# Kernel optimization log

Hardware: AMD Instinct MI355X
Metric: run time of the kernel (lower is better)

## Reference

```python
import jax, jax.numpy as jnp
import numpy as np

DIM = 2048
N_HEADS = 16
Q_LORA = 1536
KV_LORA = 512
NOPE = 128
ROPE = 64
V_DIM = 128
QK_HEAD = NOPE + ROPE
SEQ = 4096
THETA = 10000.0
EPS = 1e-6
SCALE = QK_HEAD ** -0.5  # max_seq_len==4096 not >4096, so no mscale adjustment


def rms_norm(x, w):
    return x * jax.lax.rsqrt(jnp.mean(x * x, axis=-1, keepdims=True) + EPS) * w


def rope_cos_sin(seqlen):
    inv_freq = 1.0 / THETA ** (jnp.arange(0, ROPE, 2, dtype=jnp.float32) / ROPE)  # [ROPE/2]
    t = jnp.arange(seqlen, dtype=jnp.float32)
    freqs = jnp.outer(t, inv_freq)  # [S, ROPE/2]
    return jnp.cos(freqs), jnp.sin(freqs)


def apply_rope(x, cos, sin):
    # x: (b, s, h, ROPE); pairs (x0, x1) rotated as complex mult, interleaved layout
    b, s, h, d = x.shape
    xr = x.reshape(b, s, h, d // 2, 2)
    x0, x1 = xr[..., 0], xr[..., 1]
    c = cos[None, :, None, :]
    sn = sin[None, :, None, :]
    out = jnp.stack([x0 * c - x1 * sn, x0 * sn + x1 * c], axis=-1)
    return out.reshape(b, s, h, d)


def setup_inputs() -> dict:
    key = jax.random.key(0)
    ks = jax.random.split(key, 8)
    s = lambda fan_in: 1.0 / np.sqrt(fan_in)
    return {
        "x": jax.random.normal(ks[0], (1, SEQ, DIM), jnp.float32),
        "wq_a_w": jax.random.normal(ks[1], (Q_LORA, DIM), jnp.float32) * s(DIM),
        "q_norm_w": 1.0 + 0.02 * jax.random.normal(ks[2], (Q_LORA,), jnp.float32),
        "wq_b_w": jax.random.normal(ks[3], (N_HEADS * QK_HEAD, Q_LORA), jnp.float32) * s(Q_LORA),
        "wkv_a_w": jax.random.normal(ks[4], (KV_LORA + ROPE, DIM), jnp.float32) * s(DIM),
        "kv_norm_w": 1.0 + 0.02 * jax.random.normal(ks[5], (KV_LORA,), jnp.float32),
        "wkv_b_w": jax.random.normal(ks[6], (N_HEADS * (NOPE + V_DIM), KV_LORA), jnp.float32) * s(KV_LORA),
        "wo_w": jax.random.normal(ks[7], (DIM, DIM), jnp.float32) * s(DIM),
    }


def reference(x, wq_a_w, q_norm_w, wq_b_w, wkv_a_w, kv_norm_w, wkv_b_w, wo_w):
    b, seqlen, _ = x.shape
    cos, sin = rope_cos_sin(seqlen)

    # Q path: low-rank down-proj -> RMSNorm -> up-proj
    q = rms_norm(x @ wq_a_w.T, q_norm_w) @ wq_b_w.T
    q = q.reshape(b, seqlen, N_HEADS, QK_HEAD)
    q_nope, q_pe = q[..., :NOPE], q[..., NOPE:]
    q_pe = apply_rope(q_pe, cos, sin)

    # KV path: compressed latent + decoupled rope key
    kv_a = x @ wkv_a_w.T  # (b, s, KV_LORA + ROPE)
    kv_latent, k_pe_raw = kv_a[..., :KV_LORA], kv_a[..., KV_LORA:]
    kv = rms_norm(kv_latent, kv_norm_w)               # (b, t, c)
    k_pe = apply_rope(k_pe_raw[:, :, None, :], cos, sin)[:, :, 0, :]  # (b, t, r)

    # Absorption trick: fold wkv_b's K-part into q_nope, attend against latents
    wkv_b = wkv_b_w.reshape(N_HEADS, NOPE + V_DIM, KV_LORA)
    q_abs = jnp.einsum("bshd,hdc->bshc", q_nope, wkv_b[:, :NOPE])

    scores = (jnp.einsum("bshc,btc->bsht", q_abs, kv)
              + jnp.einsum("bshr,btr->bsht", q_pe, k_pe)) * SCALE

    # causal additive mask over (s_query, t_key)
    causal = jnp.tril(jnp.ones((seqlen, seqlen), dtype=bool))
    scores = jnp.where(causal[None, :, None, :], scores, jnp.float32(-1e30))
    attn = jax.nn.softmax(scores, axis=-1)

    # post-softmax: aggregate latents, then recover V via wkv_b's V-part
    ctx = jnp.einsum("bsht,btc->bshc", attn, kv)
    v = jnp.einsum("bshc,hdc->bshd", ctx, wkv_b[:, NOPE:])  # (b, s, h, V_DIM)
    out = v.reshape(b, seqlen, N_HEADS * V_DIM) @ wo_w.T
    return out
```

## Files before the change

### kernel.cpp

```cpp
#include <hip/hip_runtime.h>

typedef unsigned short u16;
typedef __attribute__((ext_vector_type(8))) short bf16x8;
typedef __attribute__((ext_vector_type(4))) float f32x4;
typedef __attribute__((ext_vector_type(4))) unsigned short u16x4;

#define MFMA16(a, b, c) __builtin_amdgcn_mfma_f32_16x16x32_bf16((a), (b), (c), 0, 0, 0)

#define SEQ 4096
#define SCALE 0.07216878364870323f
#define LOGTHETA 9.210340371976184f

__device__ __forceinline__ u16 f2bf(float f) {
  union { float f; unsigned u; } c; c.f = f;
  unsigned u = c.u;
  unsigned r = (u + 0x7fffu + ((u >> 16) & 1u)) >> 16;
  return (u16)r;
}
__device__ __forceinline__ float bf2f(u16 b) {
  union { unsigned u; float f; } c; c.u = ((unsigned)b) << 16;
  return c.f;
}

__global__ void cvt_all(const float* __restrict__ x, const float* __restrict__ wqa,
                        const float* __restrict__ wqb, const float* __restrict__ wkva,
                        const float* __restrict__ wkvb, const float* __restrict__ wo,
                        u16* __restrict__ xb, u16* __restrict__ wqab,
                        u16* __restrict__ wqbb, u16* __restrict__ wkvab,
                        u16* __restrict__ wkvbb, u16* __restrict__ wob) {
  const int e0 = 2097152;
  const int e1 = e0 + 786432;
  const int e2 = e1 + 1179648;
  const int e3 = e2 + 294912;
  const int e4 = e3 + 524288;
  const int e5 = e4 + 1048576;
  int stride = gridDim.x * blockDim.x;
  for (int i = blockIdx.x * blockDim.x + threadIdx.x; i < e5; i += stride) {
    const float* src; u16* dst; int j;
    if (i < e0)      { src = x;    dst = xb;    j = i; }
    else if (i < e1) { src = wqa;  dst = wqab;  j = i - e0; }
    else if (i < e2) { src = wqb;  dst = wqbb;  j = i - e1; }
    else if (i < e3) { src = wkva; dst = wkvab; j = i - e2; }
    else if (i < e4) { src = wkvb; dst = wkvbb; j = i - e3; }
    else             { src = wo;   dst = wob;   j = i - e4; }
    f32x4 v = ((const f32x4*)src)[j];
    u16x4 o;
    o[0] = f2bf(v[0]); o[1] = f2bf(v[1]); o[2] = f2bf(v[2]); o[3] = f2bf(v[3]);
    ((u16x4*)dst)[j] = o;
  }
}

__global__ void trans_wkvb(const float* __restrict__ w, u16* __restrict__ wt) {
  __shared__ float tile[64][65];
  int c0 = blockIdx.x * 64;
  int d0 = blockIdx.y * 64;
  int h = blockIdx.z;
  for (int k = 0; k < 16; k++) {
    int el = threadIdx.x + k * 256;
    int r = el >> 6, c = el & 63;
    tile[r][c] = w[(h * 256 + d0 + r) * 512 + c0 + c];
  }
  __syncthreads();
  for (int k = 0; k < 16; k++) {
    int el = threadIdx.x + k * 256;
    int r = el >> 6, c = el & 63;
    wt[h * 65536 + (c0 + r) * 128 + d0 + c] = f2bf(tile[c][r]);
  }
}

__global__ void trans_vt(const u16* __restrict__ cc, u16* __restrict__ vt2) {
  __shared__ u16 tile[64][65];
  int c0 = blockIdx.x * 64;
  int t0 = blockIdx.y * 64;
  for (int k = 0; k < 16; k++) {
    int el = threadIdx.x + k * 256;
    int r = el >> 6, c = el & 63;
    tile[r][c] = cc[(t0 + r) * 2112 + 1536 + c0 + c];
  }
  __syncthreads();
  for (int k = 0; k < 16; k++) {
    int el = threadIdx.x + k * 256;
    int r = el >> 6, c = el & 63;
    int t = t0 + c;
    vt2[(t >> 5) * 16384 + (c0 + r) * 32 + (t & 31)] = tile[c][r];
  }
}

__global__ void rms_q_kernel(u16* __restrict__ cc, const float* __restrict__ w) {
  int row = blockIdx.x;
  u16* p = cc + (size_t)row * 2112;
  float vals[6];
  float ss = 0.f;
#pragma unroll
  for (int k = 0; k < 6; k++) {
    float v = bf2f(p[threadIdx.x + k * 256]);
    vals[k] = v;
    ss += v * v;
  }
  for (int m = 1; m < 64; m <<= 1) ss += __shfl_xor(ss, m);
  __shared__ float red[4];
  int wid = threadIdx.x >> 6;
  if ((threadIdx.x & 63) == 0) red[wid] = ss;
  __syncthreads();
  float tot = red[0] + red[1] + red[2] + red[3];
  float rr = rsqrtf(tot / 1536.f + 1e-6f);
#pragma unroll
  for (int k = 0; k < 6; k++) {
    int i = threadIdx.x + k * 256;
    p[i] = f2bf(vals[k] * rr * w[i]);
  }
}

__global__ void rms_kv_kernel(u16* __restrict__ cc, const float* __restrict__ w) {
  int t = blockIdx.x;
  u16* p = cc + (size_t)t * 2112 + 1536;
  float v0 = bf2f(p[threadIdx.x]);
  float v1 = bf2f(p[threadIdx.x + 256]);
  float ss = v0 * v0 + v1 * v1;
  for (int m = 1; m < 64; m <<= 1) ss += __shfl_xor(ss, m);
  __shared__ float red[4];
  int wid = threadIdx.x >> 6;
  if ((threadIdx.x & 63) == 0) red[wid] = ss;
  __syncthreads();
  float tot = red[0] + red[1] + red[2] + red[3];
  float rr = rsqrtf(tot / 512.f + 1e-6f);
  p[threadIdx.x] = f2bf(v0 * rr * w[threadIdx.x]);
  p[threadIdx.x + 256] = f2bf(v1 * rr * w[threadIdx.x + 256]);
  if (threadIdx.x < 32) {
    int i = threadIdx.x;
    float x0 = bf2f(p[512 + 2 * i]);
    float x1 = bf2f(p[512 + 2 * i + 1]);
    float invf = expf(-((float)(2 * i) / 64.f) * LOGTHETA);
    float ang = (float)t * invf;
    float cs = cosf(ang), sn = sinf(ang);
    p[512 + 2 * i] = f2bf(x0 * cs - x1 * sn);
    p[512 + 2 * i + 1] = f2bf(x0 * sn + x1 * cs);
  }
}

__global__ void rope_q_kernel(const u16* __restrict__ qb, u16* __restrict__ qcat) {
  int stride = gridDim.x * blockDim.x;
  for (int idx = blockIdx.x * blockDim.x + threadIdx.x; idx < 4096 * 512; idx += stride) {
    int s = idx >> 9;
    int r = idx & 511;
    int h = r >> 5, i = r & 31;
    float x0 = bf2f(qb[s * 3072 + h * 192 + 128 + 2 * i]);
    float x1 = bf2f(qb[s * 3072 + h * 192 + 128 + 2 * i + 1]);
    float invf = expf(-((float)(2 * i) / 64.f) * LOGTHETA);
    float ang = (float)s * invf;
    float cs = cosf(ang) * SCALE, sn = sinf(ang) * SCALE;
    qcat[s * 9216 + h * 576 + 512 + 2 * i] = f2bf(x0 * cs - x1 * sn);
    qcat[s * 9216 + h * 576 + 512 + 2 * i + 1] = f2bf(x0 * sn + x1 * cs);
  }
}

template <bool OUTF32>
__launch_bounds__(512, 2)
__global__ void gemm256(const u16* __restrict__ A, int lda,
                        const u16* __restrict__ W, int ldw,
                        void* __restrict__ Cp, int ldc, int K, float oscale,
                        int nvalid) {
  __shared__ __align__(16) u16 lds[4][16384];

  int wid = threadIdx.x >> 6, lane = threadIdx.x & 63;
  int quad = lane >> 4, l16 = lane & 15;
  int wr = wid >> 2, wc = wid & 3;
  int m0 = blockIdx.y * 256;
  int n0 = blockIdx.x * 256;

  f32x4 acc[8][4];
#pragma unroll
  for (int i = 0; i < 8; i++)
#pragma unroll
    for (int j = 0; j < 4; j++) acc[i][j] = {0.f, 0.f, 0.f, 0.f};

  const u16* sp[4];
  int soff[4];
#pragma unroll
  for (int jj = 0; jj < 4; jj++) {
    int c = jj * 8 + wid;
    soff[jj] = c * 512 + lane * 8;
    if (c < 16) {
      sp[jj] = A + (size_t)(m0 + c * 16 + l16) * lda + quad * 8;
    } else {
      int row = n0 + (c - 16) * 16 + l16;
      if (row >= nvalid) row = nvalid - 1;
      sp[jj] = W + (size_t)row * ldw + quad * 8;
    }
  }

  int nkt = K >> 5;

#pragma unroll
  for (int t = 0; t < 3; t++) {
#pragma unroll
    for (int jj = 0; jj < 4; jj++) {
      __builtin_amdgcn_global_load_lds(
          (const __attribute__((address_space(1))) unsigned int*)sp[jj],
          (__attribute__((address_space(3))) unsigned int*)&lds[t][soff[jj]], 16, 0, 0);
      sp[jj] += 32;
    }
  }

  for (int kt = 0; kt < nkt; kt++) {
    int rem = nkt - kt;
    if (rem >= 3)      asm volatile("s_waitcnt vmcnt(8)" ::: "memory");
    else if (rem == 2) asm volatile("s_waitcnt vmcnt(4)" ::: "memory");
    else               asm volatile("s_waitcnt vmcnt(0)" ::: "memory");
    __builtin_amdgcn_s_barrier();
    __builtin_amdgcn_sched_barrier(0);

    if (kt + 3 < nkt) {
#pragma unroll
      for (int jj = 0; jj < 4; jj++) {
        __builtin_amdgcn_global_load_lds(
            (const __attribute__((address_space(1))) unsigned int*)sp[jj],
            (__attribute__((address_space(3))) unsigned int*)&lds[(kt + 3) & 3][soff[jj]],
            16, 0, 0);
        sp[jj] += 32;
      }
    }

    const u16* base = &lds[kt & 3][0];
    bf16x8 a[8], b[4];
#pragma unroll
    for (int i = 0; i < 8; i++)
      a[i] = *(const bf16x8*)(base + (wr * 8 + i) * 512 + lane * 8);
#pragma unroll
    for (int j = 0; j < 4; j++)
      b[j] = *(const bf16x8*)(base + (16 + wc * 4 + j) * 512 + lane * 8);
#pragma unroll
    for (int i = 0; i < 8; i++)
#pragma unroll
      for (int j = 0; j < 4; j++) acc[i][j] = MFMA16(a[i], b[j], acc[i][j]);
  }

#pragma unroll
  for (int i = 0; i < 8; i++) {
    int row = m0 + wr * 128 + i * 16 + quad * 4;
#pragma unroll
    for (int j = 0; j < 4; j++) {
      int col = n0 + wc * 64 + j * 16 + l16;
      if (col < nvalid) {
#pragma unroll
        for (int r = 0; r < 4; r++) {
          size_t cbase = (size_t)(row + r) * ldc + col;
          if (OUTF32) ((float*)Cp)[cbase] = acc[i][j][r] * oscale;
          else        ((u16*)Cp)[cbase] = f2bf(acc[i][j][r] * oscale);
        }
      }
    }
  }
}

template <int BN, bool OUTF32>
__launch_bounds__(256)
__global__ void gemm_tiled(const u16* __restrict__ A, int lda, int az,
                           const u16* __restrict__ W, int ldw, int wz,
                           void* __restrict__ Cp, int ldc, int cz, int K, float oscale,
                           int nvalid) {
  constexpr int NCH = 8 + BN / 16;
  constexpr int NBF = BN / 32;
  __shared__ __align__(16) u16 lds[2][NCH * 512];

  int z = blockIdx.z;
  int wid = threadIdx.x >> 6, lane = threadIdx.x & 63;
  int quad = lane >> 4, l16 = lane & 15;
  int wr = wid >> 1, wc = wid & 1;
  int m0 = blockIdx.y * 128;
  int n0 = blockIdx.x * BN;

  const u16* Az = A + (size_t)z * az;
  const u16* Wz = W + (size_t)z * wz;

  f32x4 acc[4][NBF];
#pragma unroll
  for (int i = 0; i < 4; i++)
#pragma unroll
    for (int j = 0; j < NBF; j++) acc[i][j] = {0.f, 0.f, 0.f, 0.f};

#pragma unroll
  for (int jj = 0; jj < NCH / 4; jj++) {
    int c = jj * 4 + wid;
    const u16* src = (c < 8) ? (Az + (m0 + c * 16 + l16) * (size_t)lda + quad * 8)
                             : (Wz + (n0 + (c - 8) * 16 + l16) * (size_t)ldw + quad * 8);
    __builtin_amdgcn_global_load_lds(
        (const __attribute__((address_space(1))) unsigned int*)src,
        (__attribute__((address_space(3))) unsigned int*)&lds[0][c * 512], 16, 0, 0);
  }

  int buf = 0;
  for (int k0 = 0; k0 < K; k0 += 32) {
    __syncthreads();
    if (k0 + 32 < K) {
      int k1 = k0 + 32;
#pragma unroll
      for (int jj = 0; jj < NCH / 4; jj++) {
        int c = jj * 4 + wid;
        const u16* src = (c < 8) ? (Az + (m0 + c * 16 + l16) * (size_t)lda + k1 + quad * 8)
                                 : (Wz + (n0 + (c - 8) * 16 + l16) * (size_t)ldw + k1 + quad * 8);
        __builtin_amdgcn_global_load_lds(
            (const __attribute__((address_space(1))) unsigned int*)src,
            (__attribute__((address_space(3))) unsigned int*)&lds[buf ^ 1][c * 512], 16, 0, 0);
      }
    }
    const u16* base = &lds[buf][0];
    bf16x8 a[4], b[NBF];
#pragma unroll
    for (int i = 0; i < 4; i++)
      a[i] = *(const bf16x8*)(base + (wr * 4 + i) * 512 + lane * 8);
#pragma unroll
    for (int j = 0; j < NBF; j++)
      b[j] = *(const bf16x8*)(base + (8 + wc * NBF + j) * 512 + lane * 8);
#pragma unroll
    for (int i = 0; i < 4; i++)
#pragma unroll
      for (int j = 0; j < NBF; j++) acc[i][j] = MFMA16(a[i], b[j], acc[i][j]);
    buf ^= 1;
  }

#pragma unroll
  for (int i = 0; i < 4; i++) {
    int row = m0 + wr * 64 + i * 16 + quad * 4;
#pragma unroll
    for (int j = 0; j < NBF; j++) {
      int col = n0 + wc * (BN / 2) + j * 16 + l16;
      if (col < nvalid) {
#pragma unroll
        for (int r = 0; r < 4; r++) {
          size_t cbase = (size_t)z * cz + (size_t)(row + r) * ldc + col;
          if (OUTF32) ((float*)Cp)[cbase] = acc[i][j][r] * oscale;
          else        ((u16*)Cp)[cbase] = f2bf(acc[i][j][r] * oscale);
        }
      }
    }
  }
}

__launch_bounds__(512, 2)
__global__ void attn_kernel(const u16* __restrict__ qcat, const u16* __restrict__ kcat,
                            const u16* __restrict__ vt2, u16* __restrict__ ctx) {
  __shared__ __align__(16) u16 lds[2][34816];
  __shared__ __align__(16) u16 plds[8][16][40];

  int wid = threadIdx.x >> 6, lane = threadIdx.x & 63;
  int quad = lane >> 4, l16 = lane & 15;
  int bx = blockIdx.x;
  int h = bx & 15;
  int jb = 31 - (bx >> 4);
  int qb0 = jb << 7;
  int m0 = qb0 + wid * 16;

  bf16x8 q[18];
  {
    const u16* qb = qcat + (m0 + l16) * 9216 + h * 576 + quad * 8;
#pragma unroll
    for (int kk = 0; kk < 18; kk++) q[kk] = *(const bf16x8*)(qb + kk * 32);
  }

  f32x4 zero = {0.f, 0.f, 0.f, 0.f};
  f32x4 o[32];
#pragma unroll
  for (int ct = 0; ct < 32; ct++) o[ct] = zero;
  float li[4] = {0.f, 0.f, 0.f, 0.f};

  int nt = (qb0 >> 5) + 4;

  const u16* sp[9];
  int sstr[9], soff[9];
  bool sact[9];
#pragma unroll
  for (int jj = 0; jj < 9; jj++) {
    int c = jj * 8 + wid;
    sact[jj] = (c < 68);
    soff[jj] = c * 512;
    if (c < 36) {
      int kk = c >> 1, half = c & 1;
      sp[jj] = kcat + (half * 16 + l16) * 2112 + kk * 32 + quad * 8;
      sstr[jj] = 32 * 2112;
    } else {
      int ct = c - 36;
      sp[jj] = vt2 + (ct * 16 + l16) * 32 + quad * 8;
      sstr[jj] = 16384;
    }
  }

#pragma unroll
  for (int jj = 0; jj < 9; jj++) {
    if (sact[jj]) {
      __builtin_amdgcn_global_load_lds(
          (const __attribute__((address_space(1))) unsigned int*)sp[jj],
          (__attribute__((address_space(3))) unsigned int*)&lds[0][soff[jj]], 16, 0, 0);
      sp[jj] += sstr[jj];
    }
  }

  for (int ti = 0; ti < nt; ti++) {
    __syncthreads();
    int buf = ti & 1;
    if (ti + 1 < nt) {
      u16* dbase = &lds[buf ^ 1][0];
#pragma unroll
      for (int jj = 0; jj < 9; jj++) {
        if (sact[jj]) {
          __builtin_amdgcn_global_load_lds(
              (const __attribute__((address_space(1))) unsigned int*)sp[jj],
              (__attribute__((address_space(3))) unsigned int*)&dbase[soff[jj]], 16, 0, 0);
          sp[jj] += sstr[jj];
        }
      }
    }

    int t0 = ti << 5;
    if (t0 <= m0 + 15) {
      const u16* kb = &lds[buf][0];
      const u16* vb = &lds[buf][18432];
      f32x4 s0 = zero, s1 = zero;
#pragma unroll
      for (int kk = 0; kk < 18; kk++) {
        bf16x8 b0 = *(const bf16x8*)(&kb[(kk * 2 + 0) * 512 + lane * 8]);
        bf16x8 b1 = *(const bf16x8*)(&kb[(kk * 2 + 1) * 512 + lane * 8]);
        s0 = MFMA16(q[kk], b0, s0);
        s1 = MFMA16(q[kk], b1, s1);
      }
      int tc0 = t0 + l16, tc1 = t0 + 16 + l16;
#pragma unroll
      for (int r = 0; r < 4; r++) {
        int mrow = m0 + quad * 4 + r;
        float e0 = (tc0 <= mrow) ? __expf(s0[r]) : 0.f;
        float e1 = (tc1 <= mrow) ? __expf(s1[r]) : 0.f;
        li[r] += e0 + e1;
        plds[wid][quad * 4 + r][l16] = f2bf(e0);
        plds[wid][quad * 4 + r][16 + l16] = f2bf(e1);
      }
      __threadfence_block();
      bf16x8 ap = *(const bf16x8*)(&plds[wid][l16][quad * 8]);
#pragma unroll
      for (int ct = 0; ct < 32; ct++) {
        bf16x8 bv = *(const bf16x8*)(&vb[ct * 512 + lane * 8]);
        o[ct] = MFMA16(ap, bv, o[ct]);
      }
    }
  }

#pragma unroll
  for (int r = 0; r < 4; r++) {
    float s = li[r];
    s += __shfl_xor(s, 1);
    s += __shfl_xor(s, 2);
    s += __shfl_xor(s, 4);
    s += __shfl_xor(s, 8);
    li[r] = s;
  }
  f32x4 inv = {1.f / li[0], 1.f / li[1], 1.f / li[2], 1.f / li[3]};
#pragma unroll
  for (int ct = 0; ct < 32; ct++) {
    f32x4 val = o[ct] * inv;
    int base = (m0 + quad * 4) * 8192 + h * 512 + ct * 16 + l16;
    ctx[base] = f2bf(val[0]);
    ctx[base + 8192] = f2bf(val[1]);
    ctx[base + 2 * 8192] = f2bf(val[2]);
    ctx[base + 3 * 8192] = f2bf(val[3]);
  }
}

extern "C" void kernel_launch(void* const* d_in, const int* in_sizes, int n_in,
                              void* d_out, int out_size, void* d_ws, size_t ws_size,
                              hipStream_t stream) {
  const float* x = (const float*)d_in[0];
  const float* wqa = (const float*)d_in[1];
  const float* qnw = (const float*)d_in[2];
  const float* wqb = (const float*)d_in[3];
  const float* wkva = (const float*)d_in[4];
  const float* kvnw = (const float*)d_in[5];
  const float* wkvb = (const float*)d_in[6];
  const float* wo = (const float*)d_in[7];

  u16* ws = (u16*)d_ws;
  u16* XB = ws;
  u16* WQAB = ws + 8388608;
  u16* WKVAB = ws + 11534336;
  u16* WQBB = ws + 12713984;
  u16* WKVBB = ws + 17432576;
  u16* WKVBT = ws + 19529728;
  u16* WOB = ws + 20578304;
  u16* CC = ws + 24772608;
  u16* VT = ws + 33423360;
  u16* QCAT = ws + 35520512;
  u16* CTX = ws + 73269248;
  u16* QB = CTX;
  u16* VBUF = QCAT;

  dim3 blk(256);

  cvt_all<<<2048, blk, 0, stream>>>(x, wqa, wqb, wkva, wkvb, wo,
                                    XB, WQAB, WQBB, WKVAB, WKVBB, WOB);
  trans_wkvb<<<dim3(8, 2, 16), blk, 0, stream>>>(wkvb, WKVBT);

  gemm256<false><<<dim3(9, 16), dim3(512), 0, stream>>>(
      XB, 2048, WQAB, 2048, CC, 2112, 2048, 1.f, 2112);

  rms_q_kernel<<<4096, blk, 0, stream>>>(CC, qnw);
  rms_kv_kernel<<<4096, blk, 0, stream>>>(CC, kvnw);
  trans_vt<<<dim3(8, 64), blk, 0, stream>>>(CC, VT);

  gemm256<false><<<dim3(12, 16), dim3(512), 0, stream>>>(
      CC, 2112, WQBB, 1536, QB, 3072, 1536, 1.f, 3072);

  gemm_tiled<128, false><<<dim3(4, 32, 16), blk, 0, stream>>>(
      QB, 3072, 192, WKVBT, 128, 65536, QCAT, 9216, 576, 128, SCALE, 1 << 30);
  rope_q_kernel<<<2048, blk, 0, stream>>>(QB, QCAT);

  attn_kernel<<<512, dim3(512), 0, stream>>>(QCAT, CC + 1536, VT, CTX);

  gemm_tiled<128, false><<<dim3(1, 32, 16), blk, 0, stream>>>(
      CTX, 8192, 512, WKVBB + 65536, 512, 131072, VBUF, 2048, 128, 512, 1.f, 1 << 30);

  gemm256<true><<<dim3(8, 16), dim3(512), 0, stream>>>(
      VBUF, 2048, WOB, 2048, d_out, 2048, 2048, 1.f, 2048);
}
```

Measured before the change: 858.7 us.

## Unify GEMMs into batched gemm256 template, fuse RMS norms, vectorize q RoPE

Generalizes gemm256 to take a tile-width template parameter and a batch dimension, replacing gemm_tiled in the per-head GEMMs. The first projection and the output projection now use 256x128 tiles to launch more blocks and reduce padding waste. The two RMSNorm kernels are merged into one pass over each row, and the q RoPE kernel computes sincos once per position and reuses it across all 16 heads with 32-bit loads and stores. It also switches to fast __expf/__sincosf intrinsics, which may slightly change numerics.

```diff
diff --git a/kernel.cpp b/kernel.cpp
--- a/kernel.cpp
+++ b/kernel.cpp
@@ -86,106 +86,116 @@
   }
 }
 
-__global__ void rms_q_kernel(u16* __restrict__ cc, const float* __restrict__ w) {
-  int row = blockIdx.x;
-  u16* p = cc + (size_t)row * 2112;
-  float vals[6];
-  float ss = 0.f;
+__global__ void rms_qkv_kernel(u16* __restrict__ cc, const float* __restrict__ qw,
+                               const float* __restrict__ kvw) {
+  int t = blockIdx.x;
+  u16* p = cc + (size_t)t * 2112;
+  float qv[6];
+  float ssq = 0.f;
 #pragma unroll
   for (int k = 0; k < 6; k++) {
     float v = bf2f(p[threadIdx.x + k * 256]);
-    vals[k] = v;
-    ss += v * v;
-  }
-  for (int m = 1; m < 64; m <<= 1) ss += __shfl_xor(ss, m);
-  __shared__ float red[4];
+    qv[k] = v;
+    ssq += v * v;
+  }
+  float kv0 = bf2f(p[1536 + threadIdx.x]);
+  float kv1 = bf2f(p[1536 + 256 + threadIdx.x]);
+  float ssk = kv0 * kv0 + kv1 * kv1;
+  for (int m = 1; m < 64; m <<= 1) {
+    ssq += __shfl_xor(ssq, m);
+    ssk += __shfl_xor(ssk, m);
+  }
+  __shared__ float redq[4], redk[4];
   int wid = threadIdx.x >> 6;
-  if ((threadIdx.x & 63) == 0) red[wid] = ss;
+  if ((threadIdx.x & 63) == 0) { redq[wid] = ssq; redk[wid] = ssk; }
   __syncthreads();
-  float tot = red[0] + red[1] + red[2] + red[3];
-  float rr = rsqrtf(tot / 1536.f + 1e-6f);
+  float rrq = rsqrtf((redq[0] + redq[1] + redq[2] + redq[3]) / 1536.f + 1e-6f);
+  float rrk = rsqrtf((redk[0] + redk[1] + redk[2] + redk[3]) / 512.f + 1e-6f);
 #pragma unroll
   for (int k = 0; k < 6; k++) {
     int i = threadIdx.x + k * 256;
-    p[i] = f2bf(vals[k] * rr * w[i]);
-  }
-}
-
-__global__ void rms_kv_kernel(u16* __restrict__ cc, const float* __restrict__ w) {
-  int t = blockIdx.x;
-  u16* p = cc + (size_t)t * 2112 + 1536;
-  float v0 = bf2f(p[threadIdx.x]);
-  float v1 = bf2f(p[threadIdx.x + 256]);
-  float ss = v0 * v0 + v1 * v1;
-  for (int m = 1; m < 64; m <<= 1) ss += __shfl_xor(ss, m);
-  __shared__ float red[4];
-  int wid = threadIdx.x >> 6;
-  if ((threadIdx.x & 63) == 0) red[wid] = ss;
-  __syncthreads();
-  float tot = red[0] + red[1] + red[2] + red[3];
-  float rr = rsqrtf(tot / 512.f + 1e-6f);
-  p[threadIdx.x] = f2bf(v0 * rr * w[threadIdx.x]);
-  p[threadIdx.x + 256] = f2bf(v1 * rr * w[threadIdx.x + 256]);
+    p[i] = f2bf(qv[k] * rrq * qw[i]);
+  }
+  p[1536 + threadIdx.x] = f2bf(kv0 * rrk * kvw[threadIdx.x]);
+  p[1536 + 256 + threadIdx.x] = f2bf(kv1 * rrk * kvw[threadIdx.x + 256]);
   if (threadIdx.x < 32) {
     int i = threadIdx.x;
-    float x0 = bf2f(p[512 + 2 * i]);
-    float x1 = bf2f(p[512 + 2 * i + 1]);
-    float invf = expf(-((float)(2 * i) / 64.f) * LOGTHETA);
+    float x0 = bf2f(p[2048 + 2 * i]);
+    float x1 = bf2f(p[2048 + 2 * i + 1]);
+    float invf = __expf(-((float)(2 * i) / 64.f) * LOGTHETA);
     float ang = (float)t * invf;
-    float cs = cosf(ang), sn = sinf(ang);
-    p[512 + 2 * i] = f2bf(x0 * cs - x1 * sn);
-    p[512 + 2 * i + 1] = f2bf(x0 * sn + x1 * cs);
+    float cs, sn;
+    __sincosf(ang, &sn, &cs);
+    p[2048 + 2 * i] = f2bf(x0 * cs - x1 * sn);
+    p[2048 + 2 * i + 1] = f2bf(x0 * sn + x1 * cs);
   }
 }
 
 __global__ void rope_q_kernel(const u16* __restrict__ qb, u16* __restrict__ qcat) {
-  int stride = gridDim.x * blockDim.x;
-  for (int idx = blockIdx.x * blockDim.x + threadIdx.x; idx < 4096 * 512; idx += stride) {
-    int s = idx >> 9;
-    int r = idx & 511;
-    int h = r >> 5, i = r & 31;
-    float x0 = bf2f(qb[s * 3072 + h * 192 + 128 + 2 * i]);
-    float x1 = bf2f(qb[s * 3072 + h * 192 + 128 + 2 * i + 1]);
-    float invf = expf(-((float)(2 * i) / 64.f) * LOGTHETA);
-    float ang = (float)s * invf;
-    float cs = cosf(ang) * SCALE, sn = sinf(ang) * SCALE;
-    qcat[s * 9216 + h * 576 + 512 + 2 * i] = f2bf(x0 * cs - x1 * sn);
-    qcat[s * 9216 + h * 576 + 512 + 2 * i + 1] = f2bf(x0 * sn + x1 * cs);
-  }
-}
-
-template <bool OUTF32>
+  int idx = blockIdx.x * blockDim.x + threadIdx.x;
+  if (idx >= 4096 * 32) return;
+  int s = idx >> 5, i = idx & 31;
+  float invf = __expf(-((float)(2 * i) / 64.f) * LOGTHETA);
+  float ang = (float)s * invf;
+  float cs, sn;
+  __sincosf(ang, &sn, &cs);
+  cs *= SCALE; sn *= SCALE;
+  const u16* src = qb + s * 3072 + 128 + 2 * i;
+  u16* dst = qcat + s * 9216 + 512 + 2 * i;
+#pragma unroll
+  for (int h = 0; h < 16; h++) {
+    unsigned v = *(const unsigned*)(src + h * 192);
+    float x0 = bf2f((u16)(v & 0xffff));
+    float x1 = bf2f((u16)(v >> 16));
+    u16 o0 = f2bf(x0 * cs - x1 * sn);
+    u16 o1 = f2bf(x0 * sn + x1 * cs);
+    *(unsigned*)(dst + h * 576) = ((unsigned)o1 << 16) | o0;
+  }
+}
+
+template <int BN, bool OUTF32>
 __launch_bounds__(512, 2)
-__global__ void gemm256(const u16* __restrict__ A, int lda,
-                        const u16* __restrict__ W, int ldw,
-                        void* __restrict__ Cp, int ldc, int K, float oscale,
+__global__ void gemm256(const u16* __restrict__ A, int lda, int az,
+                        const u16* __restrict__ W, int ldw, int wz,
+                        void* __restrict__ Cp, int ldc, int cz, int K, float oscale,
                         int nvalid) {
-  __shared__ __align__(16) u16 lds[4][16384];
+  constexpr int NCHA = 16;
+  constexpr int NCHB = BN / 16;
+  constexpr int NCH = NCHA + NCHB;
+  constexpr int NSL = NCH / 8;
+  constexpr int WCN = (BN == 256) ? 4 : 2;
+  constexpr int AF = (BN == 256) ? 8 : 4;
+
+  __shared__ __align__(16) u16 lds[4][NCH * 512];
 
   int wid = threadIdx.x >> 6, lane = threadIdx.x & 63;
   int quad = lane >> 4, l16 = lane & 15;
-  int wr = wid >> 2, wc = wid & 3;
+  int wr = wid / WCN, wc = wid % WCN;
+  int z = blockIdx.z;
   int m0 = blockIdx.y * 256;
-  int n0 = blockIdx.x * 256;
-
-  f32x4 acc[8][4];
-#pragma unroll
-  for (int i = 0; i < 8; i++)
+  int n0 = blockIdx.x * BN;
+
+  const u16* Az = A + (size_t)z * az;
+  const u16* Wz = W + (size_t)z * wz;
+
+  f32x4 acc[AF][4];
+#pragma unroll
+  for (int i = 0; i < AF; i++)
 #pragma unroll
     for (int j = 0; j < 4; j++) acc[i][j] = {0.f, 0.f, 0.f, 0.f};
 
-  const u16* sp[4];
-  int soff[4];
-#pragma unroll
-  for (int jj = 0; jj < 4; jj++) {
+  const u16* sp[NSL];
+  int soff[NSL];
+#pragma unroll
+  for (int jj = 0; jj < NSL; jj++) {
     int c = jj * 8 + wid;
     soff[jj] = c * 512 + lane * 8;
-    if (c < 16) {
-      sp[jj] = A + (size_t)(m0 + c * 16 + l16) * lda + quad * 8;
+    if (c < NCHA) {
+      sp[jj] = Az + (size_t)(m0 + c * 16 + l16) * lda + quad * 8;
     } else {
-      int row = n0 + (c - 16) * 16 + l16;
+      int row = n0 + (c - NCHA) * 16 + l16;
       if (row >= nvalid) row = nvalid - 1;
-      sp[jj] = W + (size_t)row * ldw + quad * 8;
+      sp[jj] = Wz + (size_t)row * ldw + quad * 8;
     }
   }
 
@@ -193,26 +203,34 @@
 
 #pragma unroll
   for (int t = 0; t < 3; t++) {
-#pragma unroll
-    for (int jj = 0; jj < 4; jj++) {
-      __builtin_amdgcn_global_load_lds(
-          (const __attribute__((address_space(1))) unsigned int*)sp[jj],
-          (__attribute__((address_space(3))) unsigned int*)&lds[t][soff[jj]], 16, 0, 0);
-      sp[jj] += 32;
+    if (t < nkt) {
+#pragma unroll
+      for (int jj = 0; jj < NSL; jj++) {
+        __builtin_amdgcn_global_load_lds(
+            (const __attribute__((address_space(1))) unsigned int*)sp[jj],
+            (__attribute__((address_space(3))) unsigned int*)&lds[t][soff[jj]], 16, 0, 0);
+        sp[jj] += 32;
+      }
     }
   }
 
   for (int kt = 0; kt < nkt; kt++) {
     int rem = nkt - kt;
-    if (rem >= 3)      asm volatile("s_waitcnt vmcnt(8)" ::: "memory");
-    else if (rem == 2) asm volatile("s_waitcnt vmcnt(4)" ::: "memory");
-    else               asm volatile("s_waitcnt vmcnt(0)" ::: "memory");
+    if constexpr (BN == 256) {
+      if (rem >= 3)      asm volatile("s_waitcnt vmcnt(8)" ::: "memory");
+      else if (rem == 2) asm volatile("s_waitcnt vmcnt(4)" ::: "memory");
+      else               asm volatile("s_waitcnt vmcnt(0)" ::: "memory");
+    } else {
+      if (rem >= 3)      asm volatile("s_waitcnt vmcnt(6)" ::: "memory");
+      else if (rem == 2) asm volatile("s_waitcnt vmcnt(3)" ::: "memory");
+      else               asm volatile("s_waitcnt vmcnt(0)" ::: "memory");
+    }
     __builtin_amdgcn_s_barrier();
     __builtin_amdgcn_sched_barrier(0);
 
     if (kt + 3 < nkt) {
 #pragma unroll
-      for (int jj = 0; jj < 4; jj++) {
+      for (int jj = 0; jj < NSL; jj++) {
         __builtin_amdgcn_global_load_lds(
             (const __attribute__((address_space(1))) unsigned int*)sp[jj],
             (__attribute__((address_space(3))) unsigned int*)&lds[(kt + 3) & 3][soff[jj]],
@@ -222,109 +240,25 @@
     }
 
     const u16* base = &lds[kt & 3][0];
-    bf16x8 a[8], b[4];
-#pragma unroll
-    for (int i = 0; i < 8; i++)
-      a[i] = *(const bf16x8*)(base + (wr * 8 + i) * 512 + lane * 8);
+    bf16x8 a[AF], b[4];
+#pragma unroll
+    for (int i = 0; i < AF; i++)
+      a[i] = *(const bf16x8*)(base + (wr * AF + i) * 512 + lane * 8);
 #pragma unroll
     for (int j = 0; j < 4; j++)
-      b[j] = *(const bf16x8*)(base + (16 + wc * 4 + j) * 512 + lane * 8);
-#pragma unroll
-    for (int i = 0; i < 8; i++)
+      b[j] = *(const bf16x8*)(base + (NCHA + wc * 4 + j) * 512 + lane * 8);
+#pragma unroll
+    for (int i = 0; i < AF; i++)
 #pragma unroll
       for (int j = 0; j < 4; j++) acc[i][j] = MFMA16(a[i], b[j], acc[i][j]);
   }
 
 #pragma unroll
-  for (int i = 0; i < 8; i++) {
-    int row = m0 + wr * 128 + i * 16 + quad * 4;
+  for (int i = 0; i < AF; i++) {
+    int row = m0 + wr * (AF * 16) + i * 16 + quad * 4;
 #pragma unroll
     for (int j = 0; j < 4; j++) {
       int col = n0 + wc * 64 + j * 16 + l16;
-      if (col < nvalid) {
-#pragma unroll
-        for (int r = 0; r < 4; r++) {
-          size_t cbase = (size_t)(row + r) * ldc + col;
-          if (OUTF32) ((float*)Cp)[cbase] = acc[i][j][r] * oscale;
-          else        ((u16*)Cp)[cbase] = f2bf(acc[i][j][r] * oscale);
-        }
-      }
-    }
-  }
-}
-
-template <int BN, bool OUTF32>
-__launch_bounds__(256)
-__global__ void gemm_tiled(const u16* __restrict__ A, int lda, int az,
-                           const u16* __restrict__ W, int ldw, int wz,
-                           void* __restrict__ Cp, int ldc, int cz, int K, float oscale,
-                           int nvalid) {
-  constexpr int NCH = 8 + BN / 16;
-  constexpr int NBF = BN / 32;
-  __shared__ __align__(16) u16 lds[2][NCH * 512];
-
-  int z = blockIdx.z;
-  int wid = threadIdx.x >> 6, lane = threadIdx.x & 63;
-  int quad = lane >> 4, l16 = lane & 15;
-  int wr = wid >> 1, wc = wid & 1;
-  int m0 = blockIdx.y * 128;
-  int n0 = blockIdx.x * BN;
-
-  const u16* Az = A + (size_t)z * az;
-  const u16* Wz = W + (size_t)z * wz;
-
-  f32x4 acc[4][NBF];
-#pragma unroll
-  for (int i = 0; i < 4; i++)
-#pragma unroll
-    for (int j = 0; j < NBF; j++) acc[i][j] = {0.f, 0.f, 0.f, 0.f};
-
-#pragma unroll
-  for (int jj = 0; jj < NCH / 4; jj++) {
-    int c = jj * 4 + wid;
-    const u16* src = (c < 8) ? (Az + (m0 + c * 16 + l16) * (size_t)lda + quad * 8)
-                             : (Wz + (n0 + (c - 8) * 16 + l16) * (size_t)ldw + quad * 8);
-    __builtin_amdgcn_global_load_lds(
-        (const __attribute__((address_space(1))) unsigned int*)src,
-        (__attribute__((address_space(3))) unsigned int*)&lds[0][c * 512], 16, 0, 0);
-  }
-
-  int buf = 0;
-  for (int k0 = 0; k0 < K; k0 += 32) {
-    __syncthreads();
-    if (k0 + 32 < K) {
-      int k1 = k0 + 32;
-#pragma unroll
-      for (int jj = 0; jj < NCH / 4; jj++) {
-        int c = jj * 4 + wid;
-        const u16* src = (c < 8) ? (Az + (m0 + c * 16 + l16) * (size_t)lda + k1 + quad * 8)
-                                 : (Wz + (n0 + (c - 8) * 16 + l16) * (size_t)ldw + k1 + quad * 8);
-        __builtin_amdgcn_global_load_lds(
-            (const __attribute__((address_space(1))) unsigned int*)src,
-            (__attribute__((address_space(3))) unsigned int*)&lds[buf ^ 1][c * 512], 16, 0, 0);
-      }
-    }
-    const u16* base = &lds[buf][0];
-    bf16x8 a[4], b[NBF];
-#pragma unroll
-    for (int i = 0; i < 4; i++)
-      a[i] = *(const bf16x8*)(base + (wr * 4 + i) * 512 + lane * 8);
-#pragma unroll
-    for (int j = 0; j < NBF; j++)
-      b[j] = *(const bf16x8*)(base + (8 + wc * NBF + j) * 512 + lane * 8);
-#pragma unroll
-    for (int i = 0; i < 4; i++)
-#pragma unroll
-      for (int j = 0; j < NBF; j++) acc[i][j] = MFMA16(a[i], b[j], acc[i][j]);
-    buf ^= 1;
-  }
-
-#pragma unroll
-  for (int i = 0; i < 4; i++) {
-    int row = m0 + wr * 64 + i * 16 + quad * 4;
-#pragma unroll
-    for (int j = 0; j < NBF; j++) {
-      int col = n0 + wc * (BN / 2) + j * 16 + l16;
       if (col < nvalid) {
 #pragma unroll
         for (int r = 0; r < 4; r++) {
@@ -497,25 +431,24 @@
                                     XB, WQAB, WQBB, WKVAB, WKVBB, WOB);
   trans_wkvb<<<dim3(8, 2, 16), blk, 0, stream>>>(wkvb, WKVBT);
 
-  gemm256<false><<<dim3(9, 16), dim3(512), 0, stream>>>(
-      XB, 2048, WQAB, 2048, CC, 2112, 2048, 1.f, 2112);
-
-  rms_q_kernel<<<4096, blk, 0, stream>>>(CC, qnw);
-  rms_kv_kernel<<<4096, blk, 0, stream>>>(CC, kvnw);
+  gemm256<128, false><<<dim3(17, 16, 1), dim3(512), 0, stream>>>(
+      XB, 2048, 0, WQAB, 2048, 0, CC, 2112, 0, 2048, 1.f, 2112);
+
+  rms_qkv_kernel<<<4096, blk, 0, stream>>>(CC, qnw, kvnw);
   trans_vt<<<dim3(8, 64), blk, 0, stream>>>(CC, VT);
 
-  gemm256<false><<<dim3(12, 16), dim3(512), 0, stream>>>(
-      CC, 2112, WQBB, 1536, QB, 3072, 1536, 1.f, 3072);
-
-  gemm_tiled<128, false><<<dim3(4, 32, 16), blk, 0, stream>>>(
+  gemm256<256, false><<<dim3(12, 16, 1), dim3(512), 0, stream>>>(
+      CC, 2112, 0, WQBB, 1536, 0, QB, 3072, 0, 1536, 1.f, 1 << 30);
+
+  gemm256<128, false><<<dim3(4, 16, 16), dim3(512), 0, stream>>>(
       QB, 3072, 192, WKVBT, 128, 65536, QCAT, 9216, 576, 128, SCALE, 1 << 30);
-  rope_q_kernel<<<2048, blk, 0, stream>>>(QB, QCAT);
+  rope_q_kernel<<<512, blk, 0, stream>>>(QB, QCAT);
 
   attn_kernel<<<512, dim3(512), 0, stream>>>(QCAT, CC + 1536, VT, CTX);
 
-  gemm_tiled<128, false><<<dim3(1, 32, 16), blk, 0, stream>>>(
+  gemm256<128, false><<<dim3(1, 16, 16), dim3(512), 0, stream>>>(
       CTX, 8192, 512, WKVBB + 65536, 512, 131072, VBUF, 2048, 128, 512, 1.f, 1 << 30);
 
-  gemm256<true><<<dim3(8, 16), dim3(512), 0, stream>>>(
-      VBUF, 2048, WOB, 2048, d_out, 2048, 2048, 1.f, 2048);
-}
+  gemm256<128, true><<<dim3(16, 16, 1), dim3(512), 0, stream>>>(
+      VBUF, 2048, 0, WOB, 2048, 0, d_out, 2048, 0, 2048, 1.f, 2048);
+}
```

Result: no change. 862.4 us (+0.4%).
